# Performance work log

Measured on AMD Instinct MI355X. Metric: run time of the kernel, lower is better.

Reference implementation:

```python
import jax, jax.numpy as jnp
import numpy as np

N = 50000   # nodes
E = 800000  # edges
D = 128     # in_dim == out_dim
EPS = 1e-5  # BatchNorm eps


def setup_inputs() -> dict:
    key = jax.random.key(0)
    ks = jax.random.split(key, 4)
    x = jax.random.normal(ks[0], (N, D), dtype=jnp.float32)
    edge_index = jax.random.randint(ks[1], (2, E), 0, N, dtype=jnp.int64)
    scale = np.float32(1.0 / np.sqrt(D))
    W1 = jax.random.normal(ks[2], (D, D), dtype=jnp.float32) * scale
    W2 = jax.random.normal(ks[3], (D, D), dtype=jnp.float32) * scale
    return {
        "x": x,
        "edge_index": edge_index,
        "W1": W1,
        "b1": jnp.zeros((D,), jnp.float32),
        "W2": W2,
        "b2": jnp.zeros((D,), jnp.float32),
        "gamma": jnp.ones((D,), jnp.float32),
        "beta": jnp.zeros((D,), jnp.float32),
    }


def reference(x, edge_index, W1, b1, W2, b2, gamma, beta):
    n = x.shape[0]
    loop = jnp.arange(n, dtype=edge_index.dtype)
    src = jnp.concatenate([edge_index[0], loop])  # [E+N] with self-loops
    dst = jnp.concatenate([edge_index[1], loop])
    # symmetric GCN normalization: deg computed on A + I
    deg = jax.ops.segment_sum(jnp.ones_like(dst, jnp.float32), dst, num_segments=n)
    dis = jax.lax.rsqrt(deg)  # deg >= 1 thanks to self-loops
    ew = (dis[src] * dis[dst])[:, None]  # [E+N, 1] edge weights

    def gcn_conv(h, W, b):
        hw = h @ W  # [n, D]
        agg = jax.ops.segment_sum(hw[src] * ew, dst, num_segments=n)
        return agg + b

    # layer 1: conv -> batchnorm (batch stats) -> relu -> dropout(p=0, identity)
    h1 = gcn_conv(x, W1, b1)
    mu = jnp.mean(h1, axis=0)
    var = jnp.var(h1, axis=0)  # biased variance, as torch BatchNorm normalization
    h1 = jax.nn.relu(gamma * (h1 - mu) * jax.lax.rsqrt(var + EPS) + beta)
    # layer 2: conv; skip=True sums the stacked per-layer outputs
    h2 = gcn_conv(h1, W2, b2)
    return h1 + h2
```

## Files before the change

kernel.cpp:

```cpp
#include <hip/hip_runtime.h>

#define D 128
typedef long long i64;
typedef unsigned short u16;
typedef unsigned int u32;
typedef __attribute__((ext_vector_type(8))) short bf16x8;
typedef __attribute__((ext_vector_type(4))) float f32x4;

__device__ inline float4 fma4(float a, float4 b, float4 c) {
  c.x = fmaf(a, b.x, c.x);
  c.y = fmaf(a, b.y, c.y);
  c.z = fmaf(a, b.z, c.z);
  c.w = fmaf(a, b.w, c.w);
  return c;
}

__device__ inline float4 bnrelu4(float4 v, float4 sc, float4 sh) {
  v.x = fmaxf(fmaf(v.x, sc.x, sh.x), 0.f);
  v.y = fmaxf(fmaf(v.y, sc.y, sh.y), 0.f);
  v.z = fmaxf(fmaf(v.z, sc.z, sh.z), 0.f);
  v.w = fmaxf(fmaf(v.w, sc.w, sh.w), 0.f);
  return v;
}

__device__ inline u16 f2bf(float f) {
  union { float f; u32 u; } v; v.f = f;
  u32 r = (v.u + 0x7FFFu + ((v.u >> 16) & 1u)) >> 16;
  return (u16)r;
}

__device__ inline uint2 pk4(float4 v) {
  uint2 p;
  p.x = (u32)f2bf(v.x) | ((u32)f2bf(v.y) << 16);
  p.y = (u32)f2bf(v.z) | ((u32)f2bf(v.w) << 16);
  return p;
}

__device__ inline float4 unpk4(uint2 p) {
  float4 v;
  v.x = __uint_as_float(p.x << 16);
  v.y = __uint_as_float(p.x & 0xFFFF0000u);
  v.z = __uint_as_float(p.y << 16);
  v.w = __uint_as_float(p.y & 0xFFFF0000u);
  return v;
}

__device__ inline float4 ldbf4(const u16* __restrict__ feat, size_t row, int lane) {
  return unpk4(*(const uint2*)(feat + row * D + lane * 4));
}

__global__ void k_initdet(const unsigned* __restrict__ w, int* __restrict__ flag,
                          int* __restrict__ cnt, int n) {
  if (blockIdx.x == 0) {
    __shared__ unsigned red[256];
    unsigned v = 0;
    for (int i = threadIdx.x; i < 2048; i += 256) v |= w[2 * i + 1];
    red[threadIdx.x] = v;
    __syncthreads();
    for (int s = 128; s > 0; s >>= 1) {
      if ((int)threadIdx.x < s) red[threadIdx.x] |= red[threadIdx.x + s];
      __syncthreads();
    }
    if (threadIdx.x == 0) *flag = (red[0] == 0u) ? 1 : 0;
  } else {
    int i = (blockIdx.x - 1) * blockDim.x + threadIdx.x;
    if (i < n) cnt[i] = 0;
  }
}

__global__ void k_count(const int* __restrict__ ei32, const i64* __restrict__ ei64,
                        const int* __restrict__ flag, int e, int* __restrict__ cnt) {
  int is64 = *flag;
  for (long long i = (long long)blockIdx.x * blockDim.x + threadIdx.x; i < e;
       i += (long long)gridDim.x * blockDim.x) {
    int d = is64 ? (int)ei64[e + i] : ei32[e + i];
    atomicAdd(&cnt[d], 1);
  }
}

__global__ __launch_bounds__(1024) void k_scan1(const int* __restrict__ cnt,
                                                int* __restrict__ blocksum,
                                                float* __restrict__ dis, int n) {
  __shared__ int red[1024];
  int t = threadIdx.x;
  int i = blockIdx.x * 1024 + t;
  int c = (i < n) ? cnt[i] : 0;
  if (i < n) dis[i] = rsqrtf((float)(c + 1));
  red[t] = c;
  __syncthreads();
  for (int s = 512; s > 0; s >>= 1) {
    if (t < s) red[t] += red[t + s];
    __syncthreads();
  }
  if (t == 0) blocksum[blockIdx.x] = red[0];
}

__global__ __launch_bounds__(1024) void k_scan2(int* __restrict__ blocksum, int nb) {
  __shared__ int s[1024];
  int t = threadIdx.x;
  int v0 = (t < nb) ? blocksum[t] : 0;
  s[t] = v0;
  __syncthreads();
  for (int off = 1; off < 1024; off <<= 1) {
    int v = (t >= off) ? s[t - off] : 0;
    __syncthreads();
    s[t] += v;
    __syncthreads();
  }
  if (t < nb) blocksum[t] = s[t] - v0;
}

__global__ __launch_bounds__(1024) void k_scan3(const int* __restrict__ cnt,
                                                const int* __restrict__ blocksum,
                                                int* __restrict__ rowptr, int n) {
  __shared__ int sdata[1024];
  int t = threadIdx.x;
  int i = blockIdx.x * 1024 + t;
  int c = (i < n) ? cnt[i] : 0;
  sdata[t] = c;
  __syncthreads();
  for (int off = 1; off < 1024; off <<= 1) {
    int v = (t >= off) ? sdata[t - off] : 0;
    __syncthreads();
    sdata[t] += v;
    __syncthreads();
  }
  if (i < n) rowptr[i] = blocksum[blockIdx.x] + sdata[t] - c;
}

__global__ void k_fill(const int* __restrict__ ei32, const i64* __restrict__ ei64,
                       const int* __restrict__ flag, int e,
                       int* __restrict__ rowptr, u16* __restrict__ csr_src) {
  int is64 = *flag;
  for (long long i = (long long)blockIdx.x * blockDim.x + threadIdx.x; i < e;
       i += (long long)gridDim.x * blockDim.x) {
    int s, d;
    if (is64) { s = (int)ei64[i]; d = (int)ei64[e + i]; }
    else      { s = ei32[i];      d = ei32[e + i]; }
    int slot = atomicAdd(&rowptr[d], 1);
    csr_src[slot] = (u16)s;
  }
}

#define GR 128
#define LDK 136
template <bool BN, bool XBF>
__global__ __launch_bounds__(256) void k_gemm(const float* __restrict__ Xf,
                                              const u16* __restrict__ Xb,
                                              const float* __restrict__ W,
                                              u16* __restrict__ Ybf, int n,
                                              const float* __restrict__ scale,
                                              const float* __restrict__ shift) {
  __shared__ u16 Xl[GR * LDK];
  __shared__ u16 Wt[128 * LDK];
  int t = threadIdx.x;
  int row0 = blockIdx.x * GR;
  {
    int kk = t >> 5;
    int c4 = (t & 31) << 2;
    for (int k = kk; k < 128; k += 8) {
      float4 w = *(const float4*)&W[k * D + c4];
      Wt[(c4 + 0) * LDK + k] = f2bf(w.x);
      Wt[(c4 + 1) * LDK + k] = f2bf(w.y);
      Wt[(c4 + 2) * LDK + k] = f2bf(w.z);
      Wt[(c4 + 3) * LDK + k] = f2bf(w.w);
    }
  }
  {
    int r = t >> 5;
    int c4 = (t & 31) << 2;
    float4 sc, sh;
    if (BN) { sc = ((const float4*)scale)[t & 31]; sh = ((const float4*)shift)[t & 31]; }
    for (int rr = r; rr < GR; rr += 8) {
      int gr = row0 + rr;
      uint2 pk = {0u, 0u};
      if (gr < n) {
        if (XBF) {
          pk = *(const uint2*)&Xb[(size_t)gr * D + c4];
          if (BN) pk = pk4(bnrelu4(unpk4(pk), sc, sh));
        } else {
          float4 v = *(const float4*)&Xf[(size_t)gr * D + c4];
          if (BN) v = bnrelu4(v, sc, sh);
          pk = pk4(v);
        }
      }
      *(uint2*)&Xl[rr * LDK + c4] = pk;
    }
  }
  __syncthreads();
  int wv = t >> 6;
  int l = t & 63;
  int lg = l >> 4;
  int li = l & 15;
  int wr = wv * 32;
  f32x4 acc[2][8];
#pragma unroll
  for (int m = 0; m < 2; ++m)
#pragma unroll
    for (int nf = 0; nf < 8; ++nf)
      acc[m][nf] = (f32x4){0.f, 0.f, 0.f, 0.f};
#pragma unroll
  for (int ks = 0; ks < 4; ++ks) {
    int k0 = ks * 32 + lg * 8;
    bf16x8 a0 = *(const bf16x8*)&Xl[(wr + li) * LDK + k0];
    bf16x8 a1 = *(const bf16x8*)&Xl[(wr + 16 + li) * LDK + k0];
#pragma unroll
    for (int nf = 0; nf < 8; ++nf) {
      bf16x8 b = *(const bf16x8*)&Wt[(nf * 16 + li) * LDK + k0];
      acc[0][nf] = __builtin_amdgcn_mfma_f32_16x16x32_bf16(a0, b, acc[0][nf], 0, 0, 0);
      acc[1][nf] = __builtin_amdgcn_mfma_f32_16x16x32_bf16(a1, b, acc[1][nf], 0, 0, 0);
    }
  }
#pragma unroll
  for (int m = 0; m < 2; ++m) {
#pragma unroll
    for (int r = 0; r < 4; ++r) {
      int grow = row0 + wr + 16 * m + lg * 4 + r;
      if (grow < n) {
        u16* orow = Ybf + (size_t)grow * D;
#pragma unroll
        for (int nf = 0; nf < 8; ++nf)
          orow[nf * 16 + li] = f2bf(acc[m][nf][r]);
      }
    }
  }
}

template <bool L2>
__global__ __launch_bounds__(256) void k_gather(const u16* __restrict__ feat,
                                                const u16* __restrict__ h1bf,
                                                const float* __restrict__ bias,
                                                const float* __restrict__ dis,
                                                const int* __restrict__ rowptr,
                                                const u16* __restrict__ csr_src,
                                                float* __restrict__ outf,
                                                u16* __restrict__ outb, int n,
                                                const float* __restrict__ scale,
                                                const float* __restrict__ shift,
                                                float* __restrict__ partial) {
  __shared__ float s_l[8][128];
  __shared__ float q_l[8][128];
  int t = threadIdx.x;
  int lane = t & 31;
  int g = t >> 5;
  int ngroups = gridDim.x * 8;
  float4 s4 = {0.f, 0.f, 0.f, 0.f};
  float4 q4 = {0.f, 0.f, 0.f, 0.f};
  float4 bv = ((const float4*)bias)[lane];
  float4 sc, sh;
  if (L2) { sc = ((const float4*)scale)[lane]; sh = ((const float4*)shift)[lane]; }
  for (int r = blockIdx.x * 8 + g; r < n; r += ngroups) {
    int start = (r == 0) ? 0 : rowptr[r - 1];
    int end = rowptr[r];
    float dr = dis[r];
    float4 acc = bv;
    float4 sv = ldbf4(feat, (size_t)r, lane);
    acc = fma4(dr * dr, sv, acc);
    if (L2) {
      float4 h = bnrelu4(ldbf4(h1bf, (size_t)r, lane), sc, sh);
      acc.x += h.x; acc.y += h.y; acc.z += h.z; acc.w += h.w;
    }
    float4 acc1 = {0.f, 0.f, 0.f, 0.f};
    int j = start;
    for (; j + 4 <= end; j += 4) {
      int s0 = csr_src[j];
      int s1 = csr_src[j + 1];
      int s2 = csr_src[j + 2];
      int s3 = csr_src[j + 3];
      float w0 = dis[s0] * dr;
      float w1 = dis[s1] * dr;
      float w2 = dis[s2] * dr;
      float w3 = dis[s3] * dr;
      float4 v0 = ldbf4(feat, (size_t)s0, lane);
      float4 v1 = ldbf4(feat, (size_t)s1, lane);
      float4 v2 = ldbf4(feat, (size_t)s2, lane);
      float4 v3 = ldbf4(feat, (size_t)s3, lane);
      acc = fma4(w0, v0, acc);
      acc1 = fma4(w1, v1, acc1);
      acc = fma4(w2, v2, acc);
      acc1 = fma4(w3, v3, acc1);
    }
    for (; j < end; ++j) {
      int s0 = csr_src[j];
      float w0 = dis[s0] * dr;
      acc = fma4(w0, ldbf4(feat, (size_t)s0, lane), acc);
    }
    acc.x += acc1.x; acc.y += acc1.y; acc.z += acc1.z; acc.w += acc1.w;
    if (L2) {
      ((float4*)(outf + (size_t)r * D))[lane] = acc;
    } else {
      *(uint2*)(outb + (size_t)r * D + lane * 4) = pk4(acc);
      s4.x += acc.x; s4.y += acc.y; s4.z += acc.z; s4.w += acc.w;
      q4.x = fmaf(acc.x, acc.x, q4.x);
      q4.y = fmaf(acc.y, acc.y, q4.y);
      q4.z = fmaf(acc.z, acc.z, q4.z);
      q4.w = fmaf(acc.w, acc.w, q4.w);
    }
  }
  if (!L2) {
    *(float4*)&s_l[g][lane * 4] = s4;
    *(float4*)&q_l[g][lane * 4] = q4;
    __syncthreads();
    float v = 0.f;
    if (t < 128) {
#pragma unroll
      for (int gg = 0; gg < 8; ++gg) v += s_l[gg][t];
    } else {
#pragma unroll
      for (int gg = 0; gg < 8; ++gg) v += q_l[gg][t - 128];
    }
    partial[blockIdx.x * 256 + t] = v;
  }
}

__global__ __launch_bounds__(256) void k_bnreduce(const float* __restrict__ partial,
                                                  int nbp,
                                                  const float* __restrict__ gamma,
                                                  const float* __restrict__ beta,
                                                  float* __restrict__ scale,
                                                  float* __restrict__ shift, int n) {
  __shared__ float rs[256], rq[256];
  int c = blockIdx.x;
  int t = threadIdx.x;
  float s = 0.f, q = 0.f;
  for (int b = t; b < nbp; b += 256) {
    s += partial[b * 256 + c];
    q += partial[b * 256 + 128 + c];
  }
  rs[t] = s; rq[t] = q;
  __syncthreads();
  for (int st = 128; st > 0; st >>= 1) {
    if (t < st) { rs[t] += rs[t + st]; rq[t] += rq[t + st]; }
    __syncthreads();
  }
  if (t == 0) {
    float inv_n = 1.0f / (float)n;
    float mu = rs[0] * inv_n;
    float var = rq[0] * inv_n - mu * mu;
    float sc = gamma[c] * rsqrtf(var + 1e-5f);
    scale[c] = sc;
    shift[c] = beta[c] - mu * sc;
  }
}

extern "C" void kernel_launch(void* const* d_in, const int* in_sizes, int n_in,
                              void* d_out, int out_size, void* d_ws, size_t ws_size,
                              hipStream_t stream) {
  const float* x     = (const float*)d_in[0];
  const int*   ei32  = (const int*)d_in[1];
  const i64*   ei64  = (const i64*)d_in[1];
  const float* W1    = (const float*)d_in[2];
  const float* b1    = (const float*)d_in[3];
  const float* W2    = (const float*)d_in[4];
  const float* b2    = (const float*)d_in[5];
  const float* gamma = (const float*)d_in[6];
  const float* beta  = (const float*)d_in[7];
  float* out = (float*)d_out;

  const int n = in_sizes[0] / D;
  const int e = in_sizes[1] / 2;
  const int GB1 = 1024;

  size_t npad = ((size_t)n + 255) & ~255ULL;
  size_t epad = ((size_t)e + 255) & ~255ULL;
  char* p = (char*)d_ws;
  float* dis    = (float*)p; p += npad * 4;
  int*   cnt    = (int*)p;   p += npad * 4;
  int*   rowptr = (int*)p;   p += npad * 4;
  u16*   csr16  = (u16*)p;   p += epad * 2;
  u16*   hwbf   = (u16*)p;   p += (size_t)n * D * 2;
  u16*   h1bf   = (u16*)p;   p += (size_t)n * D * 2;
  float* partial = (float*)p; p += (size_t)GB1 * 256 * 4;
  float* scale   = (float*)p; p += D * 4;
  float* shift   = (float*)p; p += D * 4;
  int*   flag    = (int*)p;   p += 256 * 4;
  int*   blocksum = (int*)p;

  int nb256 = (n + 255) / 256;
  int eb256 = (e + 255) / 256;
  int nb1024 = (n + 1023) / 1024;
  int gb = (n + 7) / 8;
  int mb = (n + GR - 1) / GR;

  k_initdet<<<nb256 + 1, 256, 0, stream>>>((const unsigned*)d_in[1], flag, cnt, n);
  k_count<<<eb256, 256, 0, stream>>>(ei32, ei64, flag, e, cnt);
  k_scan1<<<nb1024, 1024, 0, stream>>>(cnt, blocksum, dis, n);
  k_scan2<<<1, 1024, 0, stream>>>(blocksum, nb1024);
  k_scan3<<<nb1024, 1024, 0, stream>>>(cnt, blocksum, rowptr, n);
  k_fill<<<eb256, 256, 0, stream>>>(ei32, ei64, flag, e, rowptr, csr16);

  k_gemm<false, false><<<mb, 256, 0, stream>>>(x, nullptr, W1, hwbf, n, nullptr, nullptr);
  k_gather<false><<<GB1, 256, 0, stream>>>(hwbf, nullptr, b1, dis, rowptr, csr16,
                                           nullptr, h1bf, n, nullptr, nullptr, partial);
  k_bnreduce<<<D, 256, 0, stream>>>(partial, GB1, gamma, beta, scale, shift, n);

  k_gemm<true, true><<<mb, 256, 0, stream>>>(nullptr, h1bf, W2, hwbf, n, scale, shift);
  k_gather<true><<<gb, 256, 0, stream>>>(hwbf, h1bf, b2, dis, rowptr, csr16,
                                         out, nullptr, n, scale, shift, nullptr);
}
```

Measured before the change: 309.3 us.

## Build CSR via two-level bucket sort with shared-memory atomics

```diff
diff --git a/kernel.cpp b/kernel.cpp
--- a/kernel.cpp
+++ b/kernel.cpp
@@ -6,6 +6,9 @@
 typedef unsigned int u32;
 typedef __attribute__((ext_vector_type(8))) short bf16x8;
 typedef __attribute__((ext_vector_type(4))) float f32x4;
+
+#define RPB 512
+#define CH 4096
 
 __device__ inline float4 fma4(float a, float4 b, float4 c) {
   c.x = fmaf(a, b.x, c.x);
@@ -49,96 +52,127 @@
   return unpk4(*(const uint2*)(feat + row * D + lane * 4));
 }
 
-__global__ void k_initdet(const unsigned* __restrict__ w, int* __restrict__ flag,
-                          int* __restrict__ cnt, int n) {
-  if (blockIdx.x == 0) {
-    __shared__ unsigned red[256];
-    unsigned v = 0;
-    for (int i = threadIdx.x; i < 2048; i += 256) v |= w[2 * i + 1];
-    red[threadIdx.x] = v;
+__global__ void k_detect(const unsigned* __restrict__ w, int* __restrict__ flag) {
+  __shared__ unsigned red[256];
+  unsigned v = 0;
+  for (int i = threadIdx.x; i < 2048; i += 256) v |= w[2 * i + 1];
+  red[threadIdx.x] = v;
+  __syncthreads();
+  for (int s = 128; s > 0; s >>= 1) {
+    if ((int)threadIdx.x < s) red[threadIdx.x] |= red[threadIdx.x + s];
     __syncthreads();
-    for (int s = 128; s > 0; s >>= 1) {
-      if ((int)threadIdx.x < s) red[threadIdx.x] |= red[threadIdx.x + s];
-      __syncthreads();
-    }
-    if (threadIdx.x == 0) *flag = (red[0] == 0u) ? 1 : 0;
-  } else {
-    int i = (blockIdx.x - 1) * blockDim.x + threadIdx.x;
-    if (i < n) cnt[i] = 0;
-  }
-}
-
-__global__ void k_count(const int* __restrict__ ei32, const i64* __restrict__ ei64,
-                        const int* __restrict__ flag, int e, int* __restrict__ cnt) {
+  }
+  if (threadIdx.x == 0) *flag = (red[0] == 0u) ? 1 : 0;
+}
+
+__global__ __launch_bounds__(256) void k_hist(const int* __restrict__ ei32,
+                                              const i64* __restrict__ ei64,
+                                              const int* __restrict__ flag, int e,
+                                              int nb, int* __restrict__ hist) {
+  __shared__ int h[128];
+  int c = blockIdx.x;
+  int t = threadIdx.x;
+  for (int i = t; i < nb; i += 256) h[i] = 0;
+  __syncthreads();
   int is64 = *flag;
-  for (long long i = (long long)blockIdx.x * blockDim.x + threadIdx.x; i < e;
-       i += (long long)gridDim.x * blockDim.x) {
+  long long base = (long long)c * CH;
+  long long lim = base + CH < (long long)e ? base + CH : (long long)e;
+  for (long long i = base + t; i < lim; i += 256) {
     int d = is64 ? (int)ei64[e + i] : ei32[e + i];
-    atomicAdd(&cnt[d], 1);
-  }
-}
-
-__global__ __launch_bounds__(1024) void k_scan1(const int* __restrict__ cnt,
-                                                int* __restrict__ blocksum,
-                                                float* __restrict__ dis, int n) {
-  __shared__ int red[1024];
-  int t = threadIdx.x;
-  int i = blockIdx.x * 1024 + t;
-  int c = (i < n) ? cnt[i] : 0;
-  if (i < n) dis[i] = rsqrtf((float)(c + 1));
-  red[t] = c;
-  __syncthreads();
-  for (int s = 512; s > 0; s >>= 1) {
-    if (t < s) red[t] += red[t + s];
-    __syncthreads();
-  }
-  if (t == 0) blocksum[blockIdx.x] = red[0];
-}
-
-__global__ __launch_bounds__(1024) void k_scan2(int* __restrict__ blocksum, int nb) {
-  __shared__ int s[1024];
-  int t = threadIdx.x;
-  int v0 = (t < nb) ? blocksum[t] : 0;
-  s[t] = v0;
-  __syncthreads();
-  for (int off = 1; off < 1024; off <<= 1) {
-    int v = (t >= off) ? s[t - off] : 0;
-    __syncthreads();
-    s[t] += v;
-    __syncthreads();
-  }
-  if (t < nb) blocksum[t] = s[t] - v0;
-}
-
-__global__ __launch_bounds__(1024) void k_scan3(const int* __restrict__ cnt,
-                                                const int* __restrict__ blocksum,
-                                                int* __restrict__ rowptr, int n) {
-  __shared__ int sdata[1024];
-  int t = threadIdx.x;
-  int i = blockIdx.x * 1024 + t;
-  int c = (i < n) ? cnt[i] : 0;
-  sdata[t] = c;
-  __syncthreads();
-  for (int off = 1; off < 1024; off <<= 1) {
-    int v = (t >= off) ? sdata[t - off] : 0;
-    __syncthreads();
-    sdata[t] += v;
-    __syncthreads();
-  }
-  if (i < n) rowptr[i] = blocksum[blockIdx.x] + sdata[t] - c;
-}
-
-__global__ void k_fill(const int* __restrict__ ei32, const i64* __restrict__ ei64,
-                       const int* __restrict__ flag, int e,
-                       int* __restrict__ rowptr, u16* __restrict__ csr_src) {
+    atomicAdd(&h[d >> 9], 1);
+  }
+  __syncthreads();
+  for (int i = t; i < nb; i += 256) hist[c * nb + i] = h[i];
+}
+
+__global__ __launch_bounds__(128) void k_bscan(const int* __restrict__ hist,
+                                               int nc, int nb,
+                                               int* __restrict__ chunkoff,
+                                               int* __restrict__ bucketbase) {
+  __shared__ int tot[129];
+  int b = threadIdx.x;
+  if (b < nb) {
+    int s = 0;
+    for (int c = 0; c < nc; ++c) s += hist[c * nb + b];
+    tot[b] = s;
+  }
+  __syncthreads();
+  if (b == 0) {
+    int run = 0;
+    for (int i = 0; i < nb; ++i) { int v = tot[i]; tot[i] = run; run += v; }
+    tot[nb] = run;
+  }
+  __syncthreads();
+  if (b < nb) {
+    int off = tot[b];
+    for (int c = 0; c < nc; ++c) {
+      chunkoff[c * nb + b] = off;
+      off += hist[c * nb + b];
+    }
+  }
+  if (b <= nb) bucketbase[b] = tot[b];
+}
+
+__global__ __launch_bounds__(256) void k_bin(const int* __restrict__ ei32,
+                                             const i64* __restrict__ ei64,
+                                             const int* __restrict__ flag, int e,
+                                             int nb, const int* __restrict__ chunkoff,
+                                             u32* __restrict__ pairs) {
+  __shared__ int cur[128];
+  int c = blockIdx.x;
+  int t = threadIdx.x;
+  for (int i = t; i < nb; i += 256) cur[i] = chunkoff[c * nb + i];
+  __syncthreads();
   int is64 = *flag;
-  for (long long i = (long long)blockIdx.x * blockDim.x + threadIdx.x; i < e;
-       i += (long long)gridDim.x * blockDim.x) {
+  long long base = (long long)c * CH;
+  long long lim = base + CH < (long long)e ? base + CH : (long long)e;
+  for (long long i = base + t; i < lim; i += 256) {
     int s, d;
     if (is64) { s = (int)ei64[i]; d = (int)ei64[e + i]; }
     else      { s = ei32[i];      d = ei32[e + i]; }
-    int slot = atomicAdd(&rowptr[d], 1);
-    csr_src[slot] = (u16)s;
+    int slot = atomicAdd(&cur[d >> 9], 1);
+    pairs[slot] = ((u32)(d & (RPB - 1)) << 16) | (u32)(u16)s;
+  }
+}
+
+__global__ __launch_bounds__(512) void k_csr(const u32* __restrict__ pairs,
+                                             const int* __restrict__ bucketbase,
+                                             int n, int* __restrict__ rowptr,
+                                             float* __restrict__ dis,
+                                             u16* __restrict__ csr_src) {
+  __shared__ int cnts[512];
+  __shared__ int sbuf[512];
+  __shared__ int cur[512];
+  int b = blockIdx.x;
+  int t = threadIdx.x;
+  int base = bucketbase[b];
+  int end = bucketbase[b + 1];
+  cnts[t] = 0;
+  __syncthreads();
+  for (int i = base + t; i < end; i += 512)
+    atomicAdd(&cnts[pairs[i] >> 16], 1);
+  __syncthreads();
+  int c0 = cnts[t];
+  sbuf[t] = c0;
+  __syncthreads();
+  for (int off = 1; off < 512; off <<= 1) {
+    int v = (t >= off) ? sbuf[t - off] : 0;
+    __syncthreads();
+    sbuf[t] += v;
+    __syncthreads();
+  }
+  int incl = sbuf[t];
+  int gr = b * RPB + t;
+  if (gr < n) {
+    rowptr[gr] = base + incl;
+    dis[gr] = rsqrtf((float)(c0 + 1));
+  }
+  cur[t] = incl - c0;
+  __syncthreads();
+  for (int i = base + t; i < end; i += 512) {
+    u32 p = pairs[i];
+    int slot = atomicAdd(&cur[p >> 16], 1);
+    csr_src[base + slot] = (u16)(p & 0xFFFFu);
   }
 }
 
@@ -360,34 +394,34 @@
   const int n = in_sizes[0] / D;
   const int e = in_sizes[1] / 2;
   const int GB1 = 1024;
+  const int NB = (n + RPB - 1) / RPB;
+  const int NC = (e + CH - 1) / CH;
 
   size_t npad = ((size_t)n + 255) & ~255ULL;
   size_t epad = ((size_t)e + 255) & ~255ULL;
   char* p = (char*)d_ws;
-  float* dis    = (float*)p; p += npad * 4;
-  int*   cnt    = (int*)p;   p += npad * 4;
-  int*   rowptr = (int*)p;   p += npad * 4;
-  u16*   csr16  = (u16*)p;   p += epad * 2;
-  u16*   hwbf   = (u16*)p;   p += (size_t)n * D * 2;
-  u16*   h1bf   = (u16*)p;   p += (size_t)n * D * 2;
-  float* partial = (float*)p; p += (size_t)GB1 * 256 * 4;
-  float* scale   = (float*)p; p += D * 4;
-  float* shift   = (float*)p; p += D * 4;
-  int*   flag    = (int*)p;   p += 256 * 4;
-  int*   blocksum = (int*)p;
-
-  int nb256 = (n + 255) / 256;
-  int eb256 = (e + 255) / 256;
-  int nb1024 = (n + 1023) / 1024;
+  float* dis      = (float*)p; p += npad * 4;
+  int*   rowptr   = (int*)p;   p += npad * 4;
+  u16*   csr16    = (u16*)p;   p += epad * 2;
+  u32*   pairs    = (u32*)p;   p += epad * 4;
+  int*   hist     = (int*)p;   p += (size_t)NC * NB * 4;
+  int*   chunkoff = (int*)p;   p += (size_t)NC * NB * 4;
+  int*   bucketbase = (int*)p; p += ((size_t)NB + 1 + 63) / 64 * 64 * 4;
+  u16*   hwbf     = (u16*)p;   p += (size_t)n * D * 2;
+  u16*   h1bf     = (u16*)p;   p += (size_t)n * D * 2;
+  float* partial  = (float*)p; p += (size_t)GB1 * 256 * 4;
+  float* scale    = (float*)p; p += D * 4;
+  float* shift    = (float*)p; p += D * 4;
+  int*   flag     = (int*)p;   p += 256 * 4;
+
   int gb = (n + 7) / 8;
   int mb = (n + GR - 1) / GR;
 
-  k_initdet<<<nb256 + 1, 256, 0, stream>>>((const unsigned*)d_in[1], flag, cnt, n);
-  k_count<<<eb256, 256, 0, stream>>>(ei32, ei64, flag, e, cnt);
-  k_scan1<<<nb1024, 1024, 0, stream>>>(cnt, blocksum, dis, n);
-  k_scan2<<<1, 1024, 0, stream>>>(blocksum, nb1024);
-  k_scan3<<<nb1024, 1024, 0, stream>>>(cnt, blocksum, rowptr, n);
-  k_fill<<<eb256, 256, 0, stream>>>(ei32, ei64, flag, e, rowptr, csr16);
+  k_detect<<<1, 256, 0, stream>>>((const unsigned*)d_in[1], flag);
+  k_hist<<<NC, 256, 0, stream>>>(ei32, ei64, flag, e, NB, hist);
+  k_bscan<<<1, 128, 0, stream>>>(hist, NC, NB, chunkoff, bucketbase);
+  k_bin<<<NC, 256, 0, stream>>>(ei32, ei64, flag, e, NB, chunkoff, pairs);
+  k_csr<<<NB, 512, 0, stream>>>(pairs, bucketbase, n, rowptr, dis, csr16);
 
   k_gemm<false, false><<<mb, 256, 0, stream>>>(x, nullptr, W1, hwbf, n, nullptr, nullptr);
   k_gather<false><<<GB1, 256, 0, stream>>>(hwbf, nullptr, b1, dis, rowptr, csr16,
```

After: 319.9 us. 1.03x slower.
